# Performance work log

Hardware: AMD Instinct MI355X
Metric: run time of the kernel (lower is better)

Reference implementation:

```python
import jax, jax.numpy as jnp
import numpy as np
import math

NUM_HEADS = 16

def _skew(QEr):
    # QEr: [B, H, S, S] -> pad 1 on left of last dim, reshape, drop first row
    B, H, S, _ = QEr.shape
    padded = jnp.pad(QEr, ((0, 0), (0, 0), (0, 0), (1, 0)))  # [B,H,S,S+1]
    reshaped = padded.reshape(B, H, S + 1, S)
    return reshaped[:, :, 1:, :]  # [B,H,S,S]

def setup_inputs() -> dict:
    key = jax.random.key(0)
    ks = jax.random.split(key, 8)
    B, S, D, dh = 4, 1024, 1024, 64
    x = jax.random.normal(ks[0], (B, S, D), dtype=jnp.float32)
    scale = 1.0 / math.sqrt(D)
    Wq = jax.random.normal(ks[1], (D, D), dtype=jnp.float32) * scale
    Wk = jax.random.normal(ks[2], (D, D), dtype=jnp.float32) * scale
    Wv = jax.random.normal(ks[3], (D, D), dtype=jnp.float32) * scale
    bq = jnp.zeros((D,), dtype=jnp.float32)
    bk = jnp.zeros((D,), dtype=jnp.float32)
    bv = jnp.zeros((D,), dtype=jnp.float32)
    Er = jax.random.normal(ks[4], (S, dh), dtype=jnp.float32)
    return {"x": x, "Wq": Wq, "bq": bq, "Wk": Wk, "bk": bk, "Wv": Wv, "bv": bv, "Er": Er}

def reference(x, Wq, bq, Wk, bk, Wv, bv, Er):
    B, S, D = x.shape
    H = NUM_HEADS
    dh = D // H
    # Linear projections (torch Linear: x @ W.T + b)
    q = (x @ Wq.T + bq).reshape(B, S, H, dh).transpose(0, 2, 1, 3)  # [B,H,S,dh]
    k = (x @ Wk.T + bk).reshape(B, S, H, dh).transpose(0, 2, 1, 3)
    v = (x @ Wv.T + bv).reshape(B, S, H, dh).transpose(0, 2, 1, 3)
    # Relative position term: q @ Er^T then skew (start = max_len - S = 0)
    QEr = jnp.einsum('bhsd,td->bhst', q, Er)  # [B,H,S,S]
    Srel = _skew(QEr)
    QKt = jnp.einsum('bhsd,bhtd->bhst', q, k)  # [B,H,S,S]
    attn = (QKt + Srel) / math.sqrt(dh)
    causal = jnp.tril(jnp.ones((S, S), dtype=bool))
    attn = jnp.where(causal[None, None], attn, jnp.float32(-1e6))
    attn = jax.nn.softmax(attn, axis=-1)
    out = jnp.einsum('bhst,bhtd->bhsd', attn, v)  # [B,H,S,dh]
    out = out.transpose(0, 2, 1, 3).reshape(B, S, D)
    return out  # dropout is identity in eval / p=0
```

## Files before the change

kernel.cpp:

```cpp
#include <hip/hip_runtime.h>
#include <stdint.h>

#define S_LEN 1024
#define DM 1024
#define NH 16
#define DH 64
#define NB 4

typedef unsigned short u16;
typedef __attribute__((ext_vector_type(8))) short short8;
typedef __attribute__((ext_vector_type(4))) float f32x4;
typedef __attribute__((ext_vector_type(4))) unsigned int u32x4;

__device__ __forceinline__ u16 f2bf(float f) {
  union { float f; unsigned int u; } c;
  c.f = f;
  unsigned int u = c.u;
  return (u16)((u + 0x7fffu + ((u >> 16) & 1u)) >> 16);
}

__device__ __forceinline__ void g2l16(const void* g, void* l) {
  __builtin_amdgcn_global_load_lds(
      (const __attribute__((address_space(1))) unsigned int*)(uintptr_t)g,
      (__attribute__((address_space(3))) unsigned int*)(uint32_t)(uintptr_t)l,
      16, 0, 0);
}

__device__ __forceinline__ float grp16_max(float v) {
  union { float f; int i; } c, o;
  c.f = v; o.i = __builtin_amdgcn_update_dpp(c.i, c.i, 0xB1, 0xF, 0xF, false);
  v = fmaxf(v, o.f);
  c.f = v; o.i = __builtin_amdgcn_update_dpp(c.i, c.i, 0x4E, 0xF, 0xF, false);
  v = fmaxf(v, o.f);
  c.f = v; o.i = __builtin_amdgcn_update_dpp(c.i, c.i, 0x124, 0xF, 0xF, false);
  v = fmaxf(v, o.f);
  c.f = v; o.i = __builtin_amdgcn_update_dpp(c.i, c.i, 0x128, 0xF, 0xF, false);
  v = fmaxf(v, o.f);
  return v;
}
__device__ __forceinline__ float grp16_sum(float v) {
  union { float f; int i; } c, o;
  c.f = v; o.i = __builtin_amdgcn_update_dpp(c.i, c.i, 0xB1, 0xF, 0xF, false);
  v += o.f;
  c.f = v; o.i = __builtin_amdgcn_update_dpp(c.i, c.i, 0x4E, 0xF, 0xF, false);
  v += o.f;
  c.f = v; o.i = __builtin_amdgcn_update_dpp(c.i, c.i, 0x124, 0xF, 0xF, false);
  v += o.f;
  c.f = v; o.i = __builtin_amdgcn_update_dpp(c.i, c.i, 0x128, 0xF, 0xF, false);
  v += o.f;
  return v;
}

__global__ __launch_bounds__(256) void cvt_f32_bf16(
    const float* __restrict__ x, const float* __restrict__ Wq,
    const float* __restrict__ Wk, const float* __restrict__ Wv,
    const float* __restrict__ Er, u16* __restrict__ xb,
    u16* __restrict__ Wqb, u16* __restrict__ Wkb, u16* __restrict__ Wvb,
    u16* __restrict__ Erb) {
  const size_t f = ((size_t)blockIdx.x * 256 + threadIdx.x) * 8;
  const float* src;
  u16* dst;
  size_t off;
  if (f < 4194304) { src = x; dst = xb; off = f; }
  else if (f < 5242880) { src = Wq; dst = Wqb; off = f - 4194304; }
  else if (f < 6291456) { src = Wk; dst = Wkb; off = f - 5242880; }
  else if (f < 7340032) { src = Wv; dst = Wvb; off = f - 6291456; }
  else { src = Er; dst = Erb; off = f - 7340032; }
  const float4 a = *(const float4*)(src + off);
  const float4 b = *(const float4*)(src + off + 4);
  u16 o[8] = {f2bf(a.x), f2bf(a.y), f2bf(a.z), f2bf(a.w),
              f2bf(b.x), f2bf(b.y), f2bf(b.z), f2bf(b.w)};
  *(u32x4*)(dst + off) = *(const u32x4*)o;
}

__global__ __launch_bounds__(256) void qkv_gemm(
    const u16* __restrict__ x,
    const u16* __restrict__ Wq, const float* __restrict__ bq,
    const u16* __restrict__ Wk, const float* __restrict__ bk,
    const u16* __restrict__ Wv, const float* __restrict__ bv,
    u16* __restrict__ Qo, u16* __restrict__ Ko, u16* __restrict__ Vo) {
  __shared__ __attribute__((aligned(16))) u16 Al[128 * 32];
  __shared__ __attribute__((aligned(16))) u16 Bl[128 * 32];

  const int tid = threadIdx.x;
  const int lane = tid & 63;
  const int wave = tid >> 6;
  const int z = blockIdx.z;
  const u16* W = (z == 0) ? Wq : (z == 1) ? Wk : Wv;
  const float* bias = (z == 0) ? bq : (z == 1) ? bk : bv;

  const int m0 = blockIdx.y * 128;
  const int n0 = blockIdx.x * 128;

  f32x4 acc[4][4];
  const f32x4 fzero = {0.f, 0.f, 0.f, 0.f};
#pragma unroll
  for (int i = 0; i < 4; i++)
#pragma unroll
    for (int j = 0; j < 4; j++) acc[i][j] = fzero;

  const int srow = tid >> 2;
  const int schunk = tid & 3;
  const u16* gA = x + (size_t)(m0 + srow) * DM + schunk * 8;
  const u16* gB = W + (size_t)(n0 + srow) * DM + schunk * 8;

  const int fr = lane & 15;
  const int fq = lane >> 4;
  const int wr = (wave >> 1) * 64;
  const int wc = (wave & 1) * 64;

  for (int k = 0; k < DM; k += 32) {
    g2l16(gA + k, &Al[tid * 8]);
    g2l16(gA + (size_t)64 * DM + k, &Al[2048 + tid * 8]);
    g2l16(gB + k, &Bl[tid * 8]);
    g2l16(gB + (size_t)64 * DM + k, &Bl[2048 + tid * 8]);
    __syncthreads();
    short8 a[4], b[4];
#pragma unroll
    for (int i = 0; i < 4; i++)
      a[i] = *(const short8*)&Al[(wr + i * 16 + fr) * 32 + fq * 8];
#pragma unroll
    for (int j = 0; j < 4; j++)
      b[j] = *(const short8*)&Bl[(wc + j * 16 + fr) * 32 + fq * 8];
#pragma unroll
    for (int i = 0; i < 4; i++)
#pragma unroll
      for (int j = 0; j < 4; j++)
        acc[i][j] =
            __builtin_amdgcn_mfma_f32_16x16x32_bf16(a[i], b[j], acc[i][j], 0, 0, 0);
    __syncthreads();
  }

#pragma unroll
  for (int j = 0; j < 4; j++) {
    const int n = n0 + wc + j * 16 + fr;
    const float bsv = bias[n];
    const int h = n >> 6, d = n & (DH - 1);
#pragma unroll
    for (int i = 0; i < 4; i++) {
#pragma unroll
      for (int r = 0; r < 4; r++) {
        const int m = m0 + wr + i * 16 + fq * 4 + r;
        const int bb = m >> 10, s = m & (S_LEN - 1);
        const u16 o = f2bf(acc[i][j][r] + bsv);
        if (z == 2)
          Vo[((size_t)(bb * NH + h) * DH + d) * S_LEN + s] = o;
        else if (z == 1)
          Ko[((size_t)(bb * NH + h) * S_LEN + s) * DH + d] = o;
        else
          Qo[((size_t)(bb * NH + h) * S_LEN + s) * DH + d] = o;
      }
    }
  }
}

__device__ __forceinline__ f32x4 er_frag(const u16* __restrict__ Er, int e0,
                                         int fr, int fq, short8 aq0,
                                         short8 aq1) {
  int e = e0 + fr;
  e = (e > S_LEN - 1) ? (S_LEN - 1) : e;
  const short8 b0 = *(const short8*)&Er[(size_t)e * DH + fq * 8];
  const short8 b1 = *(const short8*)&Er[(size_t)e * DH + 32 + fq * 8];
  f32x4 z = {0.f, 0.f, 0.f, 0.f};
  z = __builtin_amdgcn_mfma_f32_16x16x32_bf16(aq0, b0, z, 0, 0, 0);
  z = __builtin_amdgcn_mfma_f32_16x16x32_bf16(aq1, b1, z, 0, 0, 0);
  return z;
}

__global__ __launch_bounds__(512, 4) void attn(
    const u16* __restrict__ Q, const u16* __restrict__ K,
    const u16* __restrict__ Vt, const u16* __restrict__ Er,
    float* __restrict__ out) {
  __shared__ __attribute__((aligned(16))) u16 Kl[2][64 * 64];
  __shared__ __attribute__((aligned(16))) u16 Vl[2][64 * 64];
  __shared__ __attribute__((aligned(16))) u16 Pl[8][16 * 64];

  const int tid = threadIdx.x;
  const int lane = tid & 63;
  const int w = tid >> 6;
  const int bh = blockIdx.y;
  const int b = bh >> 4, h = bh & (NH - 1);
  const int it = (bh < 32) ? (int)blockIdx.x : 7 - (int)blockIdx.x;
  const int i0 = it * 128;
  const int jmax = i0 + 64;

  const u16* Qb = Q + (size_t)bh * S_LEN * DH;
  const char* Kb = (const char*)(K + (size_t)bh * S_LEN * DH);
  const char* Vb = (const char*)(Vt + (size_t)bh * DH * S_LEN);
  u16* Pw = Pl[w];

  const int fr = lane & 15;
  const int fq = lane >> 4;
  const f32x4 fzero = {0.f, 0.f, 0.f, 0.f};

  const int r0 = tid >> 3;
  const int ch = (tid & 7) * 16;
  const int sw = ch ^ ((r0 & 7) << 4);

  auto stage = [&](int j0, int bf) {
    g2l16(Kb + (size_t)(j0 + r0) * 128 + sw,
          (char*)&Kl[bf][0] + r0 * 128 + ch);
    g2l16(Vb + (size_t)r0 * 2048 + j0 * 2 + sw,
          (char*)&Vl[bf][0] + r0 * 128 + ch);
  };

  const int i0w = i0 + w * 16;
  const short8 aq0 = *(const short8*)&Qb[(size_t)(i0w + fr) * DH + fq * 8];
  const short8 aq1 = *(const short8*)&Qb[(size_t)(i0w + fr) * DH + 32 + fq * 8];

  float mrow[4], lrow[4];
  f32x4 accO[4];
#pragma unroll
  for (int r = 0; r < 4; r++) { mrow[r] = -3.0e38f; lrow[r] = 0.f; }
#pragma unroll
  for (int t = 0; t < 4; t++) accO[t] = fzero;

  f32x4 zzc = fzero;

  int buf = 0;
  stage(0, 0);
  __syncthreads();

  for (int j0 = 0; j0 <= jmax; j0 += 64) {
    if (j0 < jmax) stage(j0 + 64, buf ^ 1);

    int tmax = (i0w + 15 - j0) >> 4;
    if (tmax > 3) tmax = 3;

    if (tmax >= 0) {
      const int ksw = (fr & 7) << 4;
      const char* Kbase = (const char*)&Kl[buf][0];

      f32x4 sfr[4];
#pragma unroll
      for (int t = 0; t < 4; t++) sfr[t] = fzero;
      __builtin_amdgcn_s_setprio(1);
#pragma unroll
      for (int t = 0; t < 4; t++)
        if (t <= tmax) {
          const char* kr = Kbase + (t * 16 + fr) * 128;
          const short8 b0 = *(const short8*)(kr + ((fq * 16) ^ ksw));
          const short8 b1 = *(const short8*)(kr + ((64 + fq * 16) ^ ksw));
          f32x4 z = fzero;
          z = __builtin_amdgcn_mfma_f32_16x16x32_bf16(aq0, b0, z, 0, 0, 0);
          z = __builtin_amdgcn_mfma_f32_16x16x32_bf16(aq1, b1, z, 0, 0, 0);
          sfr[t] = z;
        }
      __builtin_amdgcn_s_setprio(0);

      const int eb = S_LEN - 16 - i0w + j0;
      f32x4 zz[5];
#pragma unroll
      for (int f = 0; f < 5; f++) zz[f] = fzero;
      const int f0 = (j0 == 0) ? 0 : 1;
#pragma unroll
      for (int f = 0; f < 5; f++)
        if (f >= f0 && f <= tmax + 1)
          zz[f] = er_frag(Er, eb + f * 16, fr, fq, aq0, aq1);
      if (j0 > 0) zz[0] = zzc;
      zzc = zz[4];

      float p[4][4];
#pragma unroll
      for (int r = 0; r < 4; r++) {
        const int row = fq * 4 + r;
        const int c = 15 - row + fr;
        const int src = (fq << 4) | (c & 15);
        float sh[5];
#pragma unroll
        for (int f = 0; f < 5; f++) sh[f] = __shfl(zz[f][r], src);
#pragma unroll
        for (int t = 0; t < 4; t++) {
          const float rel = (c < 16) ? sh[t] : sh[t + 1];
          float sv = (sfr[t][r] + rel) * 0.125f;
          const int jj = j0 + t * 16 + fr;
          const int ii = i0w + row;
          if (jj > ii) sv = -3.0e38f;
          p[t][r] = sv;
        }
      }

#pragma unroll
      for (int r = 0; r < 4; r++) {
        float rm = fmaxf(fmaxf(p[0][r], p[1][r]), fmaxf(p[2][r], p[3][r]));
        rm = grp16_max(rm);
        const float mnew = fmaxf(mrow[r], rm);
        const float alpha = __expf(mrow[r] - mnew);
        mrow[r] = mnew;
        float rs = 0.f;
#pragma unroll
        for (int t = 0; t < 4; t++) {
          const float e = __expf(p[t][r] - mnew);
          p[t][r] = e;
          rs += e;
        }
        rs = grp16_sum(rs);
        lrow[r] = lrow[r] * alpha + rs;
#pragma unroll
        for (int t = 0; t < 4; t++) accO[t][r] *= alpha;
      }

#pragma unroll
      for (int t = 0; t < 4; t++)
#pragma unroll
        for (int r = 0; r < 4; r++)
          Pw[(fq * 4 + r) * 64 + (((t ^ fq) << 4) + fr)] = f2bf(p[t][r]);
      __builtin_amdgcn_s_waitcnt(0xC07F);

      const int rsw = (fr >> 2) << 4;
      const short8 ap0 = *(const short8*)&Pw[fr * 64 + ((fq * 8) ^ rsw)];
      const short8 ap1 = *(const short8*)&Pw[fr * 64 + ((32 + fq * 8) ^ rsw)];

      const char* Vbase = (const char*)&Vl[buf][0];
      __builtin_amdgcn_s_setprio(1);
#pragma unroll
      for (int t = 0; t < 4; t++) {
        const char* vr = Vbase + (t * 16 + fr) * 128;
        const short8 b0 = *(const short8*)(vr + ((fq * 16) ^ ksw));
        const short8 b1 = *(const short8*)(vr + ((64 + fq * 16) ^ ksw));
        accO[t] =
            __builtin_amdgcn_mfma_f32_16x16x32_bf16(ap0, b0, accO[t], 0, 0, 0);
        accO[t] =
            __builtin_amdgcn_mfma_f32_16x16x32_bf16(ap1, b1, accO[t], 0, 0, 0);
      }
      __builtin_amdgcn_s_setprio(0);
    }

    __syncthreads();
    buf ^= 1;
  }

#pragma unroll
  for (int r = 0; r < 4; r++) {
    const float inv = 1.f / lrow[r];
    const int s = i0w + fq * 4 + r;
#pragma unroll
    for (int t = 0; t < 4; t++) {
      const int d = t * 16 + fr;
      out[((size_t)b * S_LEN + s) * DM + h * DH + d] = accO[t][r] * inv;
    }
  }
}

extern "C" void kernel_launch(void* const* d_in, const int* in_sizes, int n_in,
                              void* d_out, int out_size, void* d_ws, size_t ws_size,
                              hipStream_t stream) {
  const float* x = (const float*)d_in[0];
  const float* Wq = (const float*)d_in[1];
  const float* bq = (const float*)d_in[2];
  const float* Wk = (const float*)d_in[3];
  const float* bk = (const float*)d_in[4];
  const float* Wv = (const float*)d_in[5];
  const float* bv = (const float*)d_in[6];
  const float* Er = (const float*)d_in[7];
  float* out = (float*)d_out;

  const size_t per = (size_t)NB * NH * S_LEN * DH;
  u16* Qw = (u16*)d_ws;
  u16* Kw = Qw + per;
  u16* Vw = Kw + per;
  u16* xb = Vw + per;
  u16* Wqb = xb + per;
  u16* Wkb = Wqb + (size_t)DM * DM;
  u16* Wvb = Wkb + (size_t)DM * DM;
  u16* Erb = Wvb + (size_t)DM * DM;

  cvt_f32_bf16<<<3616, 256, 0, stream>>>(x, Wq, Wk, Wv, Er, xb, Wqb, Wkb, Wvb,
                                         Erb);
  dim3 g1(DM / 128, (NB * S_LEN) / 128, 3);
  qkv_gemm<<<g1, dim3(256), 0, stream>>>(xb, Wqb, bq, Wkb, bk, Wvb, bv, Qw, Kw,
                                         Vw);
  dim3 g2(8, NB * NH);
  attn<<<g2, dim3(512), 0, stream>>>(Qw, Kw, Vw, Erb, out);
}
```

Baseline: 188.5 us.

## Stage Er tiles in LDS ring and shrink attention blocks to 64 query rows

The attention kernel now uses 256-thread blocks covering 64 query rows, launched on a 16x64 grid, with a rotated tile-to-block mapping to even out causal work. Er rows are loaded cooperatively into a 128-row LDS ring buffer instead of being read per lane from global memory, so all waves share them. K/V staging drops from double-buffered prefetch to a single buffer loaded at the start of each iteration. This exposes load latency before every tile in exchange for more blocks and less redundant Er traffic.

```diff
diff --git a/kernel.cpp b/kernel.cpp
--- a/kernel.cpp
+++ b/kernel.cpp
@@ -154,57 +154,57 @@
   }
 }
 
-__device__ __forceinline__ f32x4 er_frag(const u16* __restrict__ Er, int e0,
-                                         int fr, int fq, short8 aq0,
-                                         short8 aq1) {
-  int e = e0 + fr;
-  e = (e > S_LEN - 1) ? (S_LEN - 1) : e;
-  const short8 b0 = *(const short8*)&Er[(size_t)e * DH + fq * 8];
-  const short8 b1 = *(const short8*)&Er[(size_t)e * DH + 32 + fq * 8];
-  f32x4 z = {0.f, 0.f, 0.f, 0.f};
-  z = __builtin_amdgcn_mfma_f32_16x16x32_bf16(aq0, b0, z, 0, 0, 0);
-  z = __builtin_amdgcn_mfma_f32_16x16x32_bf16(aq1, b1, z, 0, 0, 0);
-  return z;
-}
-
-__global__ __launch_bounds__(512, 4) void attn(
+__global__ __launch_bounds__(256, 4) void attn(
     const u16* __restrict__ Q, const u16* __restrict__ K,
     const u16* __restrict__ Vt, const u16* __restrict__ Er,
     float* __restrict__ out) {
-  __shared__ __attribute__((aligned(16))) u16 Kl[2][64 * 64];
-  __shared__ __attribute__((aligned(16))) u16 Vl[2][64 * 64];
-  __shared__ __attribute__((aligned(16))) u16 Pl[8][16 * 64];
+  __shared__ __attribute__((aligned(16))) u16 Kl[64 * 64];
+  __shared__ __attribute__((aligned(16))) u16 Vl[64 * 64];
+  __shared__ __attribute__((aligned(16))) u16 El[128 * 64];
+  __shared__ __attribute__((aligned(16))) u16 Pl[4][16 * 64];
 
   const int tid = threadIdx.x;
   const int lane = tid & 63;
   const int w = tid >> 6;
   const int bh = blockIdx.y;
   const int b = bh >> 4, h = bh & (NH - 1);
-  const int it = (bh < 32) ? (int)blockIdx.x : 7 - (int)blockIdx.x;
-  const int i0 = it * 128;
-  const int jmax = i0 + 64;
+  const int it = ((int)blockIdx.x + bh + ((bh >> 4) << 2)) & 15;
+  const int i0 = it * 64;
+  const int i0w = i0 + w * 16;
+  const int E0b = S_LEN - 64 - i0;
 
   const u16* Qb = Q + (size_t)bh * S_LEN * DH;
   const char* Kb = (const char*)(K + (size_t)bh * S_LEN * DH);
   const char* Vb = (const char*)(Vt + (size_t)bh * DH * S_LEN);
+  const char* Eb = (const char*)Er;
   u16* Pw = Pl[w];
 
   const int fr = lane & 15;
   const int fq = lane >> 4;
   const f32x4 fzero = {0.f, 0.f, 0.f, 0.f};
 
-  const int r0 = tid >> 3;
+  const int r8 = tid >> 3;
   const int ch = (tid & 7) * 16;
-  const int sw = ch ^ ((r0 & 7) << 4);
-
-  auto stage = [&](int j0, int bf) {
-    g2l16(Kb + (size_t)(j0 + r0) * 128 + sw,
-          (char*)&Kl[bf][0] + r0 * 128 + ch);
-    g2l16(Vb + (size_t)r0 * 2048 + j0 * 2 + sw,
-          (char*)&Vl[bf][0] + r0 * 128 + ch);
+
+  auto stageKV = [&](int j0) {
+#pragma unroll
+    for (int p = 0; p < 2; p++) {
+      const int row = p * 32 + r8;
+      const int sw = ch ^ ((row & 7) << 4);
+      g2l16(Kb + (size_t)(j0 + row) * 128 + sw, (char*)Kl + row * 128 + ch);
+      g2l16(Vb + (size_t)row * 2048 + j0 * 2 + sw, (char*)Vl + row * 128 + ch);
+    }
   };
-
-  const int i0w = i0 + w * 16;
+  auto stageEl = [&](int e0, int np) {
+    for (int p = 0; p < np; p++) {
+      const int e = e0 + p * 32 + r8;
+      const int slot = e & 127;
+      const int ec = (e > S_LEN - 1) ? (S_LEN - 1) : e;
+      const int sw = ch ^ ((slot & 7) << 4);
+      g2l16(Eb + (size_t)ec * 128 + sw, (char*)El + slot * 128 + ch);
+    }
+  };
+
   const short8 aq0 = *(const short8*)&Qb[(size_t)(i0w + fr) * DH + fq * 8];
   const short8 aq1 = *(const short8*)&Qb[(size_t)(i0w + fr) * DH + 32 + fq * 8];
 
@@ -216,118 +216,119 @@
   for (int t = 0; t < 4; t++) accO[t] = fzero;
 
   f32x4 zzc = fzero;
-
-  int buf = 0;
-  stage(0, 0);
-  __syncthreads();
-
-  for (int j0 = 0; j0 <= jmax; j0 += 64) {
-    if (j0 < jmax) stage(j0 + 64, buf ^ 1);
+  const int ksw = (fr & 7) << 4;
+
+  for (int j0 = 0; j0 <= i0; j0 += 64) {
+    stageKV(j0);
+    if (j0 == 0) stageEl(E0b, 4);
+    else stageEl(E0b + j0 + 64, 2);
+    __syncthreads();
 
     int tmax = (i0w + 15 - j0) >> 4;
     if (tmax > 3) tmax = 3;
 
-    if (tmax >= 0) {
-      const int ksw = (fr & 7) << 4;
-      const char* Kbase = (const char*)&Kl[buf][0];
-
-      f32x4 sfr[4];
-#pragma unroll
-      for (int t = 0; t < 4; t++) sfr[t] = fzero;
-      __builtin_amdgcn_s_setprio(1);
-#pragma unroll
-      for (int t = 0; t < 4; t++)
-        if (t <= tmax) {
-          const char* kr = Kbase + (t * 16 + fr) * 128;
-          const short8 b0 = *(const short8*)(kr + ((fq * 16) ^ ksw));
-          const short8 b1 = *(const short8*)(kr + ((64 + fq * 16) ^ ksw));
-          f32x4 z = fzero;
-          z = __builtin_amdgcn_mfma_f32_16x16x32_bf16(aq0, b0, z, 0, 0, 0);
-          z = __builtin_amdgcn_mfma_f32_16x16x32_bf16(aq1, b1, z, 0, 0, 0);
-          sfr[t] = z;
-        }
-      __builtin_amdgcn_s_setprio(0);
-
-      const int eb = S_LEN - 16 - i0w + j0;
-      f32x4 zz[5];
-#pragma unroll
-      for (int f = 0; f < 5; f++) zz[f] = fzero;
-      const int f0 = (j0 == 0) ? 0 : 1;
-#pragma unroll
-      for (int f = 0; f < 5; f++)
-        if (f >= f0 && f <= tmax + 1)
-          zz[f] = er_frag(Er, eb + f * 16, fr, fq, aq0, aq1);
-      if (j0 > 0) zz[0] = zzc;
-      zzc = zz[4];
-
-      float p[4][4];
-#pragma unroll
-      for (int r = 0; r < 4; r++) {
-        const int row = fq * 4 + r;
-        const int c = 15 - row + fr;
-        const int src = (fq << 4) | (c & 15);
-        float sh[5];
-#pragma unroll
-        for (int f = 0; f < 5; f++) sh[f] = __shfl(zz[f][r], src);
-#pragma unroll
-        for (int t = 0; t < 4; t++) {
-          const float rel = (c < 16) ? sh[t] : sh[t + 1];
-          float sv = (sfr[t][r] + rel) * 0.125f;
-          const int jj = j0 + t * 16 + fr;
-          const int ii = i0w + row;
-          if (jj > ii) sv = -3.0e38f;
-          p[t][r] = sv;
-        }
-      }
-
-#pragma unroll
-      for (int r = 0; r < 4; r++) {
-        float rm = fmaxf(fmaxf(p[0][r], p[1][r]), fmaxf(p[2][r], p[3][r]));
-        rm = grp16_max(rm);
-        const float mnew = fmaxf(mrow[r], rm);
-        const float alpha = __expf(mrow[r] - mnew);
-        mrow[r] = mnew;
-        float rs = 0.f;
-#pragma unroll
-        for (int t = 0; t < 4; t++) {
-          const float e = __expf(p[t][r] - mnew);
-          p[t][r] = e;
-          rs += e;
-        }
-        rs = grp16_sum(rs);
-        lrow[r] = lrow[r] * alpha + rs;
-#pragma unroll
-        for (int t = 0; t < 4; t++) accO[t][r] *= alpha;
-      }
-
-#pragma unroll
-      for (int t = 0; t < 4; t++)
-#pragma unroll
-        for (int r = 0; r < 4; r++)
-          Pw[(fq * 4 + r) * 64 + (((t ^ fq) << 4) + fr)] = f2bf(p[t][r]);
-      __builtin_amdgcn_s_waitcnt(0xC07F);
-
-      const int rsw = (fr >> 2) << 4;
-      const short8 ap0 = *(const short8*)&Pw[fr * 64 + ((fq * 8) ^ rsw)];
-      const short8 ap1 = *(const short8*)&Pw[fr * 64 + ((32 + fq * 8) ^ rsw)];
-
-      const char* Vbase = (const char*)&Vl[buf][0];
-      __builtin_amdgcn_s_setprio(1);
+    f32x4 sfr[4];
+#pragma unroll
+    for (int t = 0; t < 4; t++) sfr[t] = fzero;
+    __builtin_amdgcn_s_setprio(1);
+#pragma unroll
+    for (int t = 0; t < 4; t++)
+      if (t <= tmax) {
+        const char* kr = (const char*)Kl + (t * 16 + fr) * 128;
+        const short8 b0 = *(const short8*)(kr + ((fq * 16) ^ ksw));
+        const short8 b1 = *(const short8*)(kr + ((64 + fq * 16) ^ ksw));
+        f32x4 z = fzero;
+        z = __builtin_amdgcn_mfma_f32_16x16x32_bf16(aq0, b0, z, 0, 0, 0);
+        z = __builtin_amdgcn_mfma_f32_16x16x32_bf16(aq1, b1, z, 0, 0, 0);
+        sfr[t] = z;
+      }
+    __builtin_amdgcn_s_setprio(0);
+
+    const int ebs = S_LEN - 16 - i0w + j0;
+    f32x4 zz[5];
+#pragma unroll
+    for (int f = 0; f < 5; f++) zz[f] = fzero;
+    const int f0 = (j0 == 0) ? 0 : 1;
+#pragma unroll
+    for (int f = 0; f < 5; f++)
+      if (f >= f0 && f <= tmax + 1) {
+        const int slot = ((ebs + f * 16) & 127) + fr;
+        const char* er = (const char*)El + slot * 128;
+        const short8 b0 = *(const short8*)(er + ((fq * 16) ^ ksw));
+        const short8 b1 = *(const short8*)(er + ((64 + fq * 16) ^ ksw));
+        f32x4 z = fzero;
+        z = __builtin_amdgcn_mfma_f32_16x16x32_bf16(aq0, b0, z, 0, 0, 0);
+        z = __builtin_amdgcn_mfma_f32_16x16x32_bf16(aq1, b1, z, 0, 0, 0);
+        zz[f] = z;
+      }
+    if (j0 > 0) zz[0] = zzc;
+    zzc = zz[4];
+
+    float p[4][4];
+#pragma unroll
+    for (int r = 0; r < 4; r++) {
+      const int row = fq * 4 + r;
+      const int c = 15 - row + fr;
+      const int src = (fq << 4) | (c & 15);
+      float sh[5];
+#pragma unroll
+      for (int f = 0; f < 5; f++) sh[f] = __shfl(zz[f][r], src);
 #pragma unroll
       for (int t = 0; t < 4; t++) {
-        const char* vr = Vbase + (t * 16 + fr) * 128;
-        const short8 b0 = *(const short8*)(vr + ((fq * 16) ^ ksw));
-        const short8 b1 = *(const short8*)(vr + ((64 + fq * 16) ^ ksw));
-        accO[t] =
-            __builtin_amdgcn_mfma_f32_16x16x32_bf16(ap0, b0, accO[t], 0, 0, 0);
-        accO[t] =
-            __builtin_amdgcn_mfma_f32_16x16x32_bf16(ap1, b1, accO[t], 0, 0, 0);
-      }
-      __builtin_amdgcn_s_setprio(0);
-    }
+        const float rel = (c < 16) ? sh[t] : sh[t + 1];
+        float sv = (sfr[t][r] + rel) * 0.125f;
+        const int jj = j0 + t * 16 + fr;
+        const int ii = i0w + row;
+        if (jj > ii) sv = -3.0e38f;
+        p[t][r] = sv;
+      }
+    }
+
+#pragma unroll
+    for (int r = 0; r < 4; r++) {
+      float rm = fmaxf(fmaxf(p[0][r], p[1][r]), fmaxf(p[2][r], p[3][r]));
+      rm = grp16_max(rm);
+      const float mnew = fmaxf(mrow[r], rm);
+      const float alpha = __expf(mrow[r] - mnew);
+      mrow[r] = mnew;
+      float rs = 0.f;
+#pragma unroll
+      for (int t = 0; t < 4; t++) {
+        const float e = __expf(p[t][r] - mnew);
+        p[t][r] = e;
+        rs += e;
+      }
+      rs = grp16_sum(rs);
+      lrow[r] = lrow[r] * alpha + rs;
+#pragma unroll
+      for (int t = 0; t < 4; t++) accO[t][r] *= alpha;
+    }
+
+#pragma unroll
+    for (int t = 0; t < 4; t++)
+#pragma unroll
+      for (int r = 0; r < 4; r++)
+        Pw[(fq * 4 + r) * 64 + (((t ^ fq) << 4) + fr)] = f2bf(p[t][r]);
+    __builtin_amdgcn_s_waitcnt(0xC07F);
+
+    const int rsw = (fr >> 2) << 4;
+    const short8 ap0 = *(const short8*)&Pw[fr * 64 + ((fq * 8) ^ rsw)];
+    const short8 ap1 = *(const short8*)&Pw[fr * 64 + ((32 + fq * 8) ^ rsw)];
+
+    __builtin_amdgcn_s_setprio(1);
+#pragma unroll
+    for (int t = 0; t < 4; t++) {
+      const char* vr = (const char*)Vl + (t * 16 + fr) * 128;
+      const short8 b0 = *(const short8*)(vr + ((fq * 16) ^ ksw));
+      const short8 b1 = *(const short8*)(vr + ((64 + fq * 16) ^ ksw));
+      accO[t] =
+          __builtin_amdgcn_mfma_f32_16x16x32_bf16(ap0, b0, accO[t], 0, 0, 0);
+      accO[t] =
+          __builtin_amdgcn_mfma_f32_16x16x32_bf16(ap1, b1, accO[t], 0, 0, 0);
+    }
+    __builtin_amdgcn_s_setprio(0);
 
     __syncthreads();
-    buf ^= 1;
   }
 
 #pragma unroll
@@ -370,6 +371,6 @@
   dim3 g1(DM / 128, (NB * S_LEN) / 128, 3);
   qkv_gemm<<<g1, dim3(256), 0, stream>>>(xb, Wqb, bq, Wkb, bk, Wvb, bv, Qw, Kw,
                                          Vw);
-  dim3 g2(8, NB * NH);
-  attn<<<g2, dim3(512), 0, stream>>>(Qw, Kw, Vw, Erb, out);
-}
+  dim3 g2(16, NB * NH);
+  attn<<<g2, dim3(256), 0, stream>>>(Qw, Kw, Vw, Erb, out);
+}
```

Measured after the change: 174.9 us. 7.2% less time.
